# Kernel tuning notes

Measured on AMD Instinct MI355X. Metric: run time of the kernel, lower is better.

Reference implementation:

```python
import jax, jax.numpy as jnp
import numpy as np

ALPHA_F = 0.1
ALPHA_L = 1.0
ALPHA_E = 1.0
V_E = 10.0


def _conv3(y, w):
    # torch Conv1d(1,1,3,padding=1), cross-correlation with 3-tap kernel w
    yp = jnp.pad(y, ((0, 0), (1, 1)))  # [B, L+2]
    return w[0] * yp[:, :-2] + w[1] * yp[:, 1:-1] + w[2] * yp[:, 2:]


def setup_inputs() -> dict:
    key = jax.random.key(0)
    k1, k2 = jax.random.split(key)
    B, T, L = 32, 64, 8192
    x = jax.random.normal(k1, (B, T, L), dtype=jnp.float32)
    w = jax.random.normal(k2, (3,), dtype=jnp.float32) * 0.1  # learned Conv1d kernel
    return {"x": x, "w": w}


def reference(x, w):
    # x: [B, T, L]; PCNN recurrence over T steps
    B, T, L = x.shape
    df = jnp.asarray(np.exp(-ALPHA_F), dtype=x.dtype)
    dl = jnp.asarray(np.exp(-ALPHA_L), dtype=x.dtype)
    de = jnp.asarray(np.exp(-ALPHA_E), dtype=x.dtype)

    def step(carry, x_n):
        f, l, e, y = carry
        f = df * f + x_n + _conv3(y, w)
        # settled_weight=True: fixed kernel [1, 0, 1]
        yp = jnp.pad(y, ((0, 0), (1, 1)))
        l = dl * l + yp[:, :-2] + yp[:, 2:]
        u = f * (1.0 + 0.5 * l)
        e = de * e + V_E * y
        y = jax.nn.sigmoid(u - e)
        return (f, l, e, y), y

    z = jnp.zeros((B, L), dtype=x.dtype)
    e0 = jnp.full((B, L), V_E / ALPHA_E, dtype=x.dtype)
    _, ys = jax.lax.scan(step, (z, z, e0, z), jnp.swapaxes(x, 0, 1))  # ys: [T, B, L]
    return jnp.swapaxes(ys, 0, 1)  # [B, T, L]
```

## Files before the change

kernel.cpp:

```cpp
#include <hip/hip_runtime.h>
#include <hip/hip_bf16.h>


#define TT 64
#define LL 8192
#define CC 128
#define HH 64
#define NCHUNK 64

typedef float v2f __attribute__((ext_vector_type(2)));

__device__ __forceinline__ float bperm(int idx, float v) {
    return __int_as_float(__builtin_amdgcn_ds_bpermute(idx, __float_as_int(v)));
}
__device__ __forceinline__ float fsigmoid(float z) {
    return __fdividef(1.0f, 1.0f + __expf(-z));
}

__global__ __launch_bounds__(256) void pcnn4_kernel(
    const float* __restrict__ x, const float* __restrict__ wptr,
    float* __restrict__ out)
{
    const int lane = threadIdx.x & 63;
    const int tile = blockIdx.x * 4 + (threadIdx.x >> 6);
    const int chunk = tile & (NCHUNK - 1);
    const int b     = tile >> 6;

    const float w0 = wptr[0], w1 = wptr[1], w2 = wptr[2];
    const float df = 0.90483741803595957f;
    const float dl = 0.36787944117144233f;
    const float de = 0.36787944117144233f;

    const int r0 = 2 * lane;
    const int c0 = chunk * CC - HH + r0;
    const int c1 = c0 + 128;
    const bool vz0 = ((unsigned)c0 < (unsigned)LL);
    const bool vz1 = ((unsigned)c1 < (unsigned)LL);
    const int cc0 = min(max(c0, 0), LL - 2);
    const int cc1 = min(max(c1, 0), LL - 2);

    const float* xbase = x + (size_t)b * TT * LL;
    const float* xp0 = xbase + cc0;
    const float* xp1 = xbase + cc1;

    const bool lo = (lane < 32);
    float* op = out + (size_t)b * TT * LL + (lo ? c1 : c0);

    const int lm1 = ((lane + 63) & 63) << 2;
    const int lp1 = ((lane + 1) & 63) << 2;

    v2f p0[8], p1[8];
    #pragma unroll
    for (int j = 0; j < 8; ++j) {
        p0[j] = *(const v2f*)(xp0 + (size_t)j * LL);
        p1[j] = *(const v2f*)(xp1 + (size_t)j * LL);
    }

    v2f f0 = {0.f, 0.f}, f1 = {0.f, 0.f};
    v2f l0 = {0.f, 0.f}, l1 = {0.f, 0.f};
    v2f e0 = {10.f, 10.f}, e1 = {10.f, 10.f};
    v2f y0 = {0.f, 0.f}, y1 = {0.f, 0.f};

    auto step = [&](v2f xa, v2f xb) {
        float rl0 = bperm(lm1, y0.y), rl1 = bperm(lm1, y1.y);
        float rr0 = bperm(lp1, y0.x), rr1 = bperm(lp1, y1.x);
        float yl0 = (lane == 0)  ? 0.f : rl0;
        float yl1 = (lane == 0)  ? rl0 : rl1;
        float yr1 = (lane == 63) ? 0.f : rr1;
        float yr0 = (lane == 63) ? rr1 : rr0;

        f0.x = df * f0.x + xa.x + (w0 * yl0  + w1 * y0.x + w2 * y0.y);
        f0.y = df * f0.y + xa.y + (w0 * y0.x + w1 * y0.y + w2 * yr0);
        f1.x = df * f1.x + xb.x + (w0 * yl1  + w1 * y1.x + w2 * y1.y);
        f1.y = df * f1.y + xb.y + (w0 * y1.x + w1 * y1.y + w2 * yr1);
        l0.x = dl * l0.x + (yl0  + y0.y);
        l0.y = dl * l0.y + (y0.x + yr0);
        l1.x = dl * l1.x + (yl1  + y1.y);
        l1.y = dl * l1.y + (y1.x + yr1);
        float u00 = f0.x * (1.0f + 0.5f * l0.x);
        float u01 = f0.y * (1.0f + 0.5f * l0.y);
        float u10 = f1.x * (1.0f + 0.5f * l1.x);
        float u11 = f1.y * (1.0f + 0.5f * l1.y);
        e0.x = de * e0.x + 10.0f * y0.x;
        e0.y = de * e0.y + 10.0f * y0.y;
        e1.x = de * e1.x + 10.0f * y1.x;
        e1.y = de * e1.y + 10.0f * y1.y;
        y0.x = vz0 ? fsigmoid(u00 - e0.x) : 0.f;
        y0.y = vz0 ? fsigmoid(u01 - e0.y) : 0.f;
        y1.x = vz1 ? fsigmoid(u10 - e1.x) : 0.f;
        y1.y = vz1 ? fsigmoid(u11 - e1.y) : 0.f;

        v2f yst;
        yst.x = lo ? y1.x : y0.x;
        yst.y = lo ? y1.y : y0.y;
        *(v2f*)op = yst;
        op += LL;
    };

    const float* xl0 = xp0 + 8 * (size_t)LL;
    const float* xl1 = xp1 + 8 * (size_t)LL;

    for (int t = 0; t < TT; t += 8) {
        const float* a0 = (t + 16 <= TT) ? xl0 : xp0;
        const float* a1 = (t + 16 <= TT) ? xl1 : xp1;
        #pragma unroll
        for (int j = 0; j < 8; ++j) {
            step(p0[j], p1[j]);
            p0[j] = *(const v2f*)(a0 + (size_t)j * LL);
            p1[j] = *(const v2f*)(a1 + (size_t)j * LL);
        }
        xl0 += 8 * (size_t)LL;
        xl1 += 8 * (size_t)LL;
    }
}

extern "C" void kernel_launch(void* const* d_in, const int* in_sizes, int n_in,
                              void* d_out, int out_size, void* d_ws, size_t ws_size,
                              hipStream_t stream) {
    const float* x = (const float*)d_in[0];
    const float* w = (const float*)d_in[1];
    float* out = (float*)d_out;
    pcnn4_kernel<<<dim3(512), dim3(256), 0, stream>>>(x, w, out);
}
```

Before: 127.1 us.

## Stream x rows into LDS via async global_load_lds with 7-deep pipeline

Replaces the per-lane register prefetch of eight timesteps with asynchronous global-to-LDS row loads into a per-wave 8-slot ring buffer, kept 7 rows ahead and paced by explicit vmcnt waits. Each wave loads one contiguous 256-float row per timestep, which removes the duplicated halo loads and the register pressure of the prefetch arrays. Output stores become nontemporal. The cost is LDS traffic for every input read and hand-tuned waitcnt values, which would be wrong if the compiler counts the stores or reorders memory operations differently.

```diff
diff --git a/kernel.cpp b/kernel.cpp
--- a/kernel.cpp
+++ b/kernel.cpp
@@ -10,6 +10,13 @@
 
 typedef float v2f __attribute__((ext_vector_type(2)));
 
+__device__ __forceinline__ void async_row_load(const float* g, float* l) {
+    __builtin_amdgcn_global_load_lds(
+        (const __attribute__((address_space(1))) unsigned int*)g,
+        (__attribute__((address_space(3))) unsigned int*)l, 16, 0, 0);
+}
+#define WAIT_VM(n) __builtin_amdgcn_s_waitcnt(0x0F70 | (n))
+
 __device__ __forceinline__ float bperm(int idx, float v) {
     return __int_as_float(__builtin_amdgcn_ds_bpermute(idx, __float_as_int(v)));
 }
@@ -17,12 +24,15 @@
     return __fdividef(1.0f, 1.0f + __expf(-z));
 }
 
-__global__ __launch_bounds__(256) void pcnn4_kernel(
+__global__ __launch_bounds__(256) void pcnn6_kernel(
     const float* __restrict__ x, const float* __restrict__ wptr,
     float* __restrict__ out)
 {
+    __shared__ __align__(16) float xs[4][8][256];
+
     const int lane = threadIdx.x & 63;
-    const int tile = blockIdx.x * 4 + (threadIdx.x >> 6);
+    const int w    = threadIdx.x >> 6;
+    const int tile = blockIdx.x * 4 + w;
     const int chunk = tile & (NCHUNK - 1);
     const int b     = tile >> 6;
 
@@ -32,29 +42,25 @@
     const float de = 0.36787944117144233f;
 
     const int r0 = 2 * lane;
-    const int c0 = chunk * CC - HH + r0;
+    const int gbase = chunk * CC - HH;
+    const int c0 = gbase + r0;
     const int c1 = c0 + 128;
     const bool vz0 = ((unsigned)c0 < (unsigned)LL);
     const bool vz1 = ((unsigned)c1 < (unsigned)LL);
-    const int cc0 = min(max(c0, 0), LL - 2);
-    const int cc1 = min(max(c1, 0), LL - 2);
+
+    const int cb = min(max(gbase, 0), LL - 256);
+    const int sh = gbase - cb;
+    const int i0 = min(max(r0 + sh, 0), 254);
+    const int i1 = min(max(r0 + 128 + sh, 0), 254);
 
     const float* xbase = x + (size_t)b * TT * LL;
-    const float* xp0 = xbase + cc0;
-    const float* xp1 = xbase + cc1;
+    const float* xg = xbase + cb + 4 * lane;
 
     const bool lo = (lane < 32);
     float* op = out + (size_t)b * TT * LL + (lo ? c1 : c0);
 
     const int lm1 = ((lane + 63) & 63) << 2;
     const int lp1 = ((lane + 1) & 63) << 2;
-
-    v2f p0[8], p1[8];
-    #pragma unroll
-    for (int j = 0; j < 8; ++j) {
-        p0[j] = *(const v2f*)(xp0 + (size_t)j * LL);
-        p1[j] = *(const v2f*)(xp1 + (size_t)j * LL);
-    }
 
     v2f f0 = {0.f, 0.f}, f1 = {0.f, 0.f};
     v2f l0 = {0.f, 0.f}, l1 = {0.f, 0.f};
@@ -93,24 +99,37 @@
         v2f yst;
         yst.x = lo ? y1.x : y0.x;
         yst.y = lo ? y1.y : y0.y;
-        *(v2f*)op = yst;
+        __builtin_nontemporal_store(yst, (v2f*)op);
         op += LL;
     };
 
-    const float* xl0 = xp0 + 8 * (size_t)LL;
-    const float* xl1 = xp1 + 8 * (size_t)LL;
+    auto consume_and_issue = [&](int j, int r) {
+        v2f xa = *(const v2f*)&xs[w][j][i0];
+        v2f xb = *(const v2f*)&xs[w][j][i1];
+        step(xa, xb);
+        const float* g = (r < TT) ? (xg + (size_t)r * LL) : xg;
+        async_row_load(g, &xs[w][(j + 7) & 7][0]);
+    };
 
-    for (int t = 0; t < TT; t += 8) {
-        const float* a0 = (t + 16 <= TT) ? xl0 : xp0;
-        const float* a1 = (t + 16 <= TT) ? xl1 : xp1;
+    #pragma unroll
+    for (int j = 0; j < 7; ++j)
+        async_row_load(xg + (size_t)j * LL, &xs[w][j][0]);
+
+    WAIT_VM(6);  consume_and_issue(0, 7);
+    WAIT_VM(7);  consume_and_issue(1, 8);
+    WAIT_VM(8);  consume_and_issue(2, 9);
+    WAIT_VM(9);  consume_and_issue(3, 10);
+    WAIT_VM(10); consume_and_issue(4, 11);
+    WAIT_VM(11); consume_and_issue(5, 12);
+    WAIT_VM(12); consume_and_issue(6, 13);
+    WAIT_VM(12); consume_and_issue(7, 14);
+
+    for (int t = 8; t < TT; t += 8) {
         #pragma unroll
         for (int j = 0; j < 8; ++j) {
-            step(p0[j], p1[j]);
-            p0[j] = *(const v2f*)(a0 + (size_t)j * LL);
-            p1[j] = *(const v2f*)(a1 + (size_t)j * LL);
+            WAIT_VM(12);
+            consume_and_issue(j, t + j + 7);
         }
-        xl0 += 8 * (size_t)LL;
-        xl1 += 8 * (size_t)LL;
     }
 }
 
@@ -120,5 +139,5 @@
     const float* x = (const float*)d_in[0];
     const float* w = (const float*)d_in[1];
     float* out = (float*)d_out;
-    pcnn4_kernel<<<dim3(512), dim3(256), 0, stream>>>(x, w, out);
+    pcnn6_kernel<<<dim3(512), dim3(256), 0, stream>>>(x, w, out);
 }
```

After: 155.9 us. +22.7%, slower.
